# Kernel optimization log

Measured on AMD Instinct MI355X. Metric: run time of the kernel, lower is better.

Reference implementation:

```python
import jax, jax.numpy as jnp
import numpy as np

N, E, F, H, G = 50000, 1600000, 128, 128, 64
EPS = 1e-5  # BatchNorm eps


def setup_inputs() -> dict:
    key = jax.random.key(0)
    ks = jax.random.split(key, 16)
    x = jax.random.normal(ks[0], (N, F), dtype=jnp.float32)
    edge_index = jax.random.randint(ks[1], (2, E), 0, N, dtype=jnp.int64)
    batch = jnp.sort(jax.random.randint(ks[2], (N,), 0, G, dtype=jnp.int64))
    inp = {
        'x': x, 'edge_index': edge_index, 'batch': batch,
        'W1': jax.random.normal(ks[3], (F, H), dtype=jnp.float32) / np.sqrt(F),
        'b1': jnp.zeros((H,), jnp.float32),
        'bn1_gamma': jax.random.uniform(ks[4], (H,), jnp.float32, 0.5, 1.5),
        'bn1_beta': jax.random.normal(ks[5], (H,), jnp.float32) * 0.1,
        'bn1_mean': jax.random.normal(ks[6], (H,), jnp.float32) * 0.1,
        'bn1_var': jax.random.uniform(ks[7], (H,), jnp.float32, 0.5, 1.5),
        'W2': jax.random.normal(ks[8], (H, H), dtype=jnp.float32) / np.sqrt(H),
        'b2': jnp.zeros((H,), jnp.float32),
        'bn2_gamma': jax.random.uniform(ks[9], (H,), jnp.float32, 0.5, 1.5),
        'bn2_beta': jax.random.normal(ks[10], (H,), jnp.float32) * 0.1,
        'bn2_mean': jax.random.normal(ks[11], (H,), jnp.float32) * 0.1,
        'bn2_var': jax.random.uniform(ks[12], (H,), jnp.float32, 0.5, 1.5),
        'att_w': jax.random.normal(ks[13], (H, 1), dtype=jnp.float32) / np.sqrt(H),
        'cls_w': jax.random.normal(ks[14], (1, H), dtype=jnp.float32) / np.sqrt(H),
        'cls_b': jnp.zeros((1,), jnp.float32),
    }
    return inp


def gcn_conv(h, W, b, src, dst, n):
    # PyG GCNConv: linear, add self-loops, symmetric D^{-1/2}(A+I)D^{-1/2} aggregation, bias.
    hw = h @ W                                   # [n, H]
    loops = jnp.arange(n, dtype=src.dtype)
    s = jnp.concatenate([src, loops])
    d = jnp.concatenate([dst, loops])
    deg = jax.ops.segment_sum(jnp.ones_like(d, dtype=hw.dtype), d, num_segments=n)
    dis = jnp.where(deg > 0, jax.lax.rsqrt(deg), 0.0)
    norm = dis[s] * dis[d]                       # [E+n]
    msgs = hw[s] * norm[:, None]                 # gather + scale (memory-bound)
    return jax.ops.segment_sum(msgs, d, num_segments=n) + b


def batch_norm(h, gamma, beta, mean, var):
    return (h - mean) * gamma * jax.lax.rsqrt(var + EPS) + beta


def reference(x, edge_index, batch, W1, b1, bn1_gamma, bn1_beta, bn1_mean, bn1_var,
              W2, b2, bn2_gamma, bn2_beta, bn2_mean, bn2_var, att_w, cls_w, cls_b):
    n = x.shape[0]
    src, dst = edge_index[0], edge_index[1]
    # eval mode: dropout and edge-dropout are no-ops; BN uses running stats
    h = gcn_conv(x, W1, b1, src, dst, n)
    h = jax.nn.relu(batch_norm(h, bn1_gamma, bn1_beta, bn1_mean, bn1_var))
    h = gcn_conv(h, W2, b2, src, dst, n)
    h = jax.nn.relu(batch_norm(h, bn2_gamma, bn2_beta, bn2_mean, bn2_var))
    att = jax.nn.sigmoid(h @ att_w)              # [n, 1]
    g = jax.ops.segment_sum(h * att, batch, num_segments=G)  # [G, H]
    logits = g @ cls_w.T + cls_b                 # [G, 1]
    return logits, att
```

## Files before the change

### kernel.cpp

```cpp
#include <hip/hip_runtime.h>
#include <math.h>

#define NN 50000
#define HID 128
#define NG 64
#define BN_EPS 1e-5f

typedef __attribute__((ext_vector_type(8))) short short8;
typedef __attribute__((ext_vector_type(4))) float f32x4;

__device__ inline unsigned pack_bf2(float a, float b) {
    union { float f; unsigned u; } ua, ub;
    ua.f = a; ub.f = b;
    unsigned x = ua.u, y = ub.u;
    x += 0x7fffu + ((x >> 16) & 1u);
    y += 0x7fffu + ((y >> 16) & 1u);
    return (x >> 16) | (y & 0xffff0000u);
}
__device__ inline unsigned short bf16_1(float x) {
    union { float f; unsigned u; } v;
    v.f = x;
    unsigned r = v.u + 0x7fffu + ((v.u >> 16) & 1u);
    return (unsigned short)(r >> 16);
}
__device__ inline float2 unpack_bf2(unsigned v) {
    union { unsigned u; float f; } a, b;
    a.u = v << 16;
    b.u = v & 0xffff0000u;
    return make_float2(a.f, b.f);
}

#define NBKT 256
#define ETILE 8192
#define CAP   8192

__global__ __launch_bounds__(256) void k_distribute(const int* __restrict__ src,
                                                    const int* __restrict__ dst,
                                                    int* __restrict__ bcurP,
                                                    unsigned* __restrict__ bpacked,
                                                    const float* __restrict__ W1,
                                                    const float* __restrict__ W2,
                                                    unsigned short* __restrict__ wt1,
                                                    unsigned short* __restrict__ wt2,
                                                    int etiles, int E, int K) {
    if ((int)blockIdx.x >= etiles) {
        int b2 = blockIdx.x - etiles;
        int k = b2 & 127;
        const float* W = (b2 < 128) ? W1 : W2;
        unsigned short* wt = (b2 < 128) ? wt1 : wt2;
        int c = threadIdx.x;
        if (c < 128) wt[c * 128 + k] = bf16_1(W[k * 128 + c]);
        return;
    }
    __shared__ int h[NBKT];
    int t = threadIdx.x;
    h[t] = 0;
    __syncthreads();
    int base = blockIdx.x * ETILE;
    for (int i = 0; i < ETILE / 256; ++i) {
        int e = base + i * 256 + t;
        if (e < E) atomicAdd(&h[dst[e] / K], 1);
    }
    __syncthreads();
    int c = h[t];
    int my = (c > 0) ? atomicAdd(&bcurP[t * 16], c) : 0;
    __syncthreads();
    h[t] = my;
    __syncthreads();
    for (int i = 0; i < ETILE / 256; ++i) {
        int e = base + i * 256 + t;
        if (e < E) {
            int d = dst[e];
            int bkt = d / K;
            int p = atomicAdd(&h[bkt], 1);
            bpacked[(size_t)bkt * CAP + p] = ((unsigned)d << 16) | (unsigned)src[e];
        }
    }
}

__global__ __launch_bounds__(256) void k_bucket_csr(const unsigned* __restrict__ bpacked,
                                                    const int* __restrict__ bcurP,
                                                    int* __restrict__ row_ptr,
                                                    int* __restrict__ degA,
                                                    float* __restrict__ dis,
                                                    int* __restrict__ col_idx,
                                                    const float* __restrict__ cls_b,
                                                    float* __restrict__ logits,
                                                    int n, int K) {
    __shared__ int cnt[NBKT];
    __shared__ int sA[NBKT];
    __shared__ int cur[NBKT];
    int t = threadIdx.x;
    int b = blockIdx.x;
    if (b == 0 && t < NG) logits[t] = cls_b[0];
    int node0 = b * K;
    int nn = n - node0;
    if (nn > K) nn = K;
    if (nn < 0) nn = 0;
    int e0 = b * CAP;
    int e1 = e0 + bcurP[b * 16];
    cnt[t] = 0;
    __syncthreads();
    for (int e = e0 + t; e < e1; e += 256) {
        int ld = (int)(bpacked[e] >> 16) - node0;
        atomicAdd(&cnt[ld], 1);
    }
    __syncthreads();
    int c = cnt[t];
    sA[t] = c;
    __syncthreads();
    for (int off = 1; off < NBKT; off <<= 1) {
        int v = (t >= off) ? sA[t - off] : 0;
        __syncthreads();
        sA[t] += v;
        __syncthreads();
    }
    int rp = e0 + sA[t] - c;
    cur[t] = rp;
    if (t < nn) {
        row_ptr[node0 + t] = rp;
        degA[node0 + t] = c;
        dis[node0 + t] = rsqrtf((float)(c + 1));
    }
    __syncthreads();
    for (int e = e0 + t; e < e1; e += 256) {
        unsigned v = bpacked[e];
        int ld = (int)(v >> 16) - node0;
        int p = atomicAdd(&cur[ld], 1);
        col_idx[p] = (int)(v & 0xFFFFu);
    }
}


#define ASTR 136

__global__ __launch_bounds__(256) void k_gemm_mfma(const void* __restrict__ inp,
                                                   const unsigned short* __restrict__ wt,
                                                   const float* __restrict__ dis,
                                                   unsigned short* __restrict__ outb,
                                                   int n, int fmt) {
    __shared__ unsigned short A[64][ASTR];
    int t = threadIdx.x;
    int row0 = blockIdx.x * 64;

    if (fmt == 0) {
        const float* in = (const float*)inp;
        #pragma unroll
        for (int i = 0; i < 8; ++i) {
            int idx = t + i * 256;
            int r = idx >> 5;
            int c4 = (idx & 31) * 4;
            float4 v = make_float4(0.f, 0.f, 0.f, 0.f);
            if (row0 + r < n) v = *(const float4*)&in[(size_t)(row0 + r) * 128 + c4];
            uint2 p;
            p.x = pack_bf2(v.x, v.y);
            p.y = pack_bf2(v.z, v.w);
            *(uint2*)&A[r][c4] = p;
        }
    } else {
        const unsigned short* in = (const unsigned short*)inp;
        #pragma unroll
        for (int i = 0; i < 4; ++i) {
            int idx = t + i * 256;
            int r = idx >> 4;
            int c8 = (idx & 15) * 8;
            uint4 v = make_uint4(0, 0, 0, 0);
            if (row0 + r < n) v = *(const uint4*)&in[(size_t)(row0 + r) * 128 + c8];
            *(uint4*)&A[r][c8] = v;
        }
    }
    __syncthreads();

    int lane = t & 63;
    int wave = t >> 6;
    int m = lane & 15;
    int quad = lane >> 4;
    int r0 = wave * 16;

    short8 a[4];
    #pragma unroll
    for (int kt = 0; kt < 4; ++kt)
        a[kt] = *(const short8*)&A[r0 + m][kt * 32 + quad * 8];

    f32x4 acc[8];
    #pragma unroll
    for (int ct = 0; ct < 8; ++ct) acc[ct] = (f32x4){0.f, 0.f, 0.f, 0.f};

    short8 bcur[4], bnxt[4];
    {
        const unsigned short* wb = &wt[(size_t)m * 128 + quad * 8];
        #pragma unroll
        for (int kt = 0; kt < 4; ++kt) bcur[kt] = *(const short8*)(wb + kt * 32);
    }
    #pragma unroll
    for (int ct = 0; ct < 8; ++ct) {
        if (ct < 7) {
            const unsigned short* wb = &wt[(size_t)((ct + 1) * 16 + m) * 128 + quad * 8];
            #pragma unroll
            for (int kt = 0; kt < 4; ++kt) bnxt[kt] = *(const short8*)(wb + kt * 32);
        }
        #pragma unroll
        for (int kt = 0; kt < 4; ++kt)
            acc[ct] = __builtin_amdgcn_mfma_f32_16x16x32_bf16(a[kt], bcur[kt], acc[ct], 0, 0, 0);
        #pragma unroll
        for (int kt = 0; kt < 4; ++kt) bcur[kt] = bnxt[kt];
    }

    int gr = row0 + r0 + quad * 4;
    float ds[4];
    #pragma unroll
    for (int reg = 0; reg < 4; ++reg)
        ds[reg] = (gr + reg < n) ? dis[gr + reg] : 0.f;

    __syncthreads();
    #pragma unroll
    for (int ct = 0; ct < 8; ++ct) {
        int col = ct * 16 + m;
        #pragma unroll
        for (int reg = 0; reg < 4; ++reg)
            A[r0 + quad * 4 + reg][col] = bf16_1(acc[ct][reg] * ds[reg]);
    }
    __syncthreads();
    #pragma unroll
    for (int i = 0; i < 4; ++i) {
        int idx = t + i * 256;
        int r = idx >> 4;
        int c8 = (idx & 15) * 8;
        int grow = row0 + r;
        if (grow < n)
            *(uint4*)&outb[(size_t)grow * 128 + c8] = *(const uint4*)&A[r][c8];
    }
}


__device__ inline void gather4wide(const unsigned short* __restrict__ hwsb,
                                   const int* __restrict__ col_idx,
                                   int e0, int deg, int md,
                                   int sl, int part, bool active,
                                   float* acc8) {
    int cidx = (active && sl < deg) ? col_idx[e0 + sl] : 0;
    for (int it0 = 0; it0 < md; it0 += 16) {
        int nx = it0 + 16;
        int cidx_next = (active && (nx + sl) < deg && nx < md) ? col_idx[e0 + nx + sl] : 0;
        uint4 vv[16];
        #pragma unroll
        for (int j = 0; j < 16; ++j) {
            int s = __shfl(cidx, (part << 4) + j);
            vv[j] = (it0 + j < deg)
                        ? *(const uint4*)(hwsb + ((size_t)s << 7) + (sl << 3))
                        : make_uint4(0, 0, 0, 0);
        }
        #pragma unroll
        for (int j = 0; j < 16; ++j) {
            const unsigned* w = (const unsigned*)&vv[j];
            #pragma unroll
            for (int i2 = 0; i2 < 4; ++i2) {
                float2 f = unpack_bf2(w[i2]);
                acc8[2 * i2]     += f.x;
                acc8[2 * i2 + 1] += f.y;
            }
        }
        cidx = cidx_next;
    }
}


__global__ __launch_bounds__(256) void k_agg_bn_relu(const unsigned short* __restrict__ hwsb,
                                                     const int* __restrict__ row_ptr,
                                                     const int* __restrict__ degA,
                                                     const int* __restrict__ col_idx,
                                                     const float* __restrict__ dis,
                                                     const float* __restrict__ bias,
                                                     const float* __restrict__ gamma,
                                                     const float* __restrict__ beta,
                                                     const float* __restrict__ mean,
                                                     const float* __restrict__ var,
                                                     unsigned short* __restrict__ outh, int n) {
    int t = threadIdx.x;
    int wave = t >> 6, lane = t & 63;
    int sl = lane & 15, part = lane >> 4;
    int d = blockIdx.x * 16 + wave * 4 + part;
    bool active = (d < n);
    int e0 = 0, deg = 0;
    if (active) {
        e0 = row_ptr[d];
        deg = degA[d];
    }
    int md = deg;
    md = max(md, __shfl_xor(md, 16));
    md = max(md, __shfl_xor(md, 32));

    float acc8[8] = {0, 0, 0, 0, 0, 0, 0, 0};
    gather4wide(hwsb, col_idx, e0, deg, md, sl, part, active, acc8);
    if (!active) return;

    {
        uint4 v = *(const uint4*)(hwsb + ((size_t)d << 7) + (sl << 3));
        const unsigned* w = (const unsigned*)&v;
        #pragma unroll
        for (int i2 = 0; i2 < 4; ++i2) {
            float2 f = unpack_bf2(w[i2]);
            acc8[2 * i2]     += f.x;
            acc8[2 * i2 + 1] += f.y;
        }
    }
    float dd = dis[d];
    int f0 = sl << 3;
    unsigned outw[4];
    #pragma unroll
    for (int i2 = 0; i2 < 4; ++i2) {
        int f = f0 + 2 * i2;
        float2 bv = *(const float2*)&bias[f];
        float2 gm = *(const float2*)&gamma[f];
        float2 bt = *(const float2*)&beta[f];
        float2 mn = *(const float2*)&mean[f];
        float2 vr = *(const float2*)&var[f];
        float vx = acc8[2 * i2] * dd + bv.x;
        float vy = acc8[2 * i2 + 1] * dd + bv.y;
        float sx = gm.x * rsqrtf(vr.x + BN_EPS);
        float sy = gm.y * rsqrtf(vr.y + BN_EPS);
        float rx = fmaxf((vx - mn.x) * sx + bt.x, 0.f);
        float ry = fmaxf((vy - mn.y) * sy + bt.y, 0.f);
        outw[i2] = pack_bf2(rx, ry);
    }
    *(uint4*)(outh + ((size_t)d << 7) + (sl << 3)) = *(uint4*)outw;
}


__global__ __launch_bounds__(256) void k_agg2_att_logit(const unsigned short* __restrict__ hwsb,
                                                        const int* __restrict__ row_ptr,
                                                        const int* __restrict__ degA,
                                                        const int* __restrict__ col_idx,
                                                        const float* __restrict__ dis,
                                                        const float* __restrict__ bias,
                                                        const float* __restrict__ gamma,
                                                        const float* __restrict__ beta,
                                                        const float* __restrict__ mean,
                                                        const float* __restrict__ var,
                                                        const int* __restrict__ batch,
                                                        const float* __restrict__ att_w,
                                                        const float* __restrict__ cls_w,
                                                        float* __restrict__ att_out,
                                                        float* __restrict__ logits, int n) {
    __shared__ int   sg[16];
    __shared__ float sv[16];
    int t = threadIdx.x;
    int wave = t >> 6, lane = t & 63;
    int sl = lane & 15, part = lane >> 4;
    int d = blockIdx.x * 16 + wave * 4 + part;
    bool active = (d < n);
    int e0 = 0, deg = 0;
    if (active) {
        e0 = row_ptr[d];
        deg = degA[d];
    }
    int md = deg;
    md = max(md, __shfl_xor(md, 16));
    md = max(md, __shfl_xor(md, 32));

    float acc8[8] = {0, 0, 0, 0, 0, 0, 0, 0};
    gather4wide(hwsb, col_idx, e0, deg, md, sl, part, active, acc8);

    int g = -1;
    float contrib = 0.f;
    float p = 0.f, q = 0.f;
    if (active) {
        uint4 v = *(const uint4*)(hwsb + ((size_t)d << 7) + (sl << 3));
        const unsigned* w = (const unsigned*)&v;
        #pragma unroll
        for (int i2 = 0; i2 < 4; ++i2) {
            float2 f = unpack_bf2(w[i2]);
            acc8[2 * i2]     += f.x;
            acc8[2 * i2 + 1] += f.y;
        }
        float dd = dis[d];
        int f0 = sl << 3;
        #pragma unroll
        for (int i2 = 0; i2 < 4; ++i2) {
            int f = f0 + 2 * i2;
            float2 bv = *(const float2*)&bias[f];
            float2 gm = *(const float2*)&gamma[f];
            float2 bt = *(const float2*)&beta[f];
            float2 mn = *(const float2*)&mean[f];
            float2 vr = *(const float2*)&var[f];
            float vx = acc8[2 * i2] * dd + bv.x;
            float vy = acc8[2 * i2 + 1] * dd + bv.y;
            float sx = gm.x * rsqrtf(vr.x + BN_EPS);
            float sy = gm.y * rsqrtf(vr.y + BN_EPS);
            float rx = fmaxf((vx - mn.x) * sx + bt.x, 0.f);
            float ry = fmaxf((vy - mn.y) * sy + bt.y, 0.f);
            float2 aw = *(const float2*)&att_w[f];
            float2 cw = *(const float2*)&cls_w[f];
            p += rx * aw.x + ry * aw.y;
            q += rx * cw.x + ry * cw.y;
        }
    }
    #pragma unroll
    for (int off = 1; off < 16; off <<= 1) {
        p += __shfl_xor(p, off);
        q += __shfl_xor(q, off);
    }
    if (active) {
        float a = 1.f / (1.f + expf(-p));
        if (sl == 0) att_out[d] = a;
        g = batch[d];
        contrib = a * q;
    }
    if (sl == 0) {
        sg[wave * 4 + part] = g;
        sv[wave * 4 + part] = contrib;
    }
    __syncthreads();
    if (t == 0) {
        int cur = -1;
        float acc = 0.f;
        #pragma unroll
        for (int i = 0; i < 16; ++i) {
            int gi = sg[i];
            if (gi < 0) continue;
            if (gi != cur) {
                if (cur >= 0) atomicAdd(&logits[cur], acc);
                cur = gi;
                acc = 0.f;
            }
            acc += sv[i];
        }
        if (cur >= 0) atomicAdd(&logits[cur], acc);
    }
}


extern "C" void kernel_launch(void* const* d_in, const int* in_sizes, int n_in,
                              void* d_out, int out_size, void* d_ws, size_t ws_size,
                              hipStream_t stream) {
    const float* x   = (const float*)d_in[0];
    const int*   ei  = (const int*)d_in[1];
    const int*   bat = (const int*)d_in[2];
    const float* W1  = (const float*)d_in[3];
    const float* b1  = (const float*)d_in[4];
    const float* g1  = (const float*)d_in[5];
    const float* bt1 = (const float*)d_in[6];
    const float* mn1 = (const float*)d_in[7];
    const float* vr1 = (const float*)d_in[8];
    const float* W2  = (const float*)d_in[9];
    const float* b2  = (const float*)d_in[10];
    const float* g2  = (const float*)d_in[11];
    const float* bt2 = (const float*)d_in[12];
    const float* mn2 = (const float*)d_in[13];
    const float* vr2 = (const float*)d_in[14];
    const float* attw = (const float*)d_in[15];
    const float* clsw = (const float*)d_in[16];
    const float* clsb = (const float*)d_in[17];

    int E = in_sizes[1] / 2;
    int n = in_sizes[2];
    const int* src = ei;
    const int* dst = ei + E;
    int K = (n + NBKT - 1) / NBKT;

    char* ws = (char*)d_ws;
    auto alloc = [&](size_t bytes) {
        void* p = (void*)ws;
        ws += (bytes + 255) & ~(size_t)255;
        return p;
    };
    int*            bcurP   = (int*)alloc(NBKT * 16 * 4);
    unsigned*       bpacked = (unsigned*)alloc((size_t)NBKT * CAP * 4);
    int*            row_ptr = (int*)alloc((size_t)n * 4);
    int*            degA    = (int*)alloc((size_t)n * 4);
    int*            col_idx = (int*)alloc((size_t)NBKT * CAP * 4);
    float*          dis     = (float*)alloc((size_t)n * 4);
    unsigned short* hwsb    = (unsigned short*)alloc((size_t)n * 128 * 2);
    unsigned short* h1b     = (unsigned short*)alloc((size_t)n * 128 * 2);
    unsigned short* wt1     = (unsigned short*)alloc(128 * 128 * 2);
    unsigned short* wt2     = (unsigned short*)alloc(128 * 128 * 2);

    float* out = (float*)d_out;
    int etiles = (E + ETILE - 1) / ETILE;
    int gb = (n + 63) / 64;
    int ab = (n + 15) / 16;

    hipMemsetAsync(bcurP, 0, NBKT * 16 * 4, stream);
    k_distribute<<<etiles + 256, 256, 0, stream>>>(src, dst, bcurP, bpacked,
                                                   W1, W2, wt1, wt2, etiles, E, K);
    k_bucket_csr<<<NBKT, 256, 0, stream>>>(bpacked, bcurP, row_ptr, degA, dis,
                                           col_idx, clsb, out, n, K);

    k_gemm_mfma<<<gb, 256, 0, stream>>>(x, wt1, dis, hwsb, n, 0);
    k_agg_bn_relu<<<ab, 256, 0, stream>>>(hwsb, row_ptr, degA, col_idx, dis,
                                          b1, g1, bt1, mn1, vr1, h1b, n);
    k_gemm_mfma<<<gb, 256, 0, stream>>>(h1b, wt2, dis, hwsb, n, 1);
    k_agg2_att_logit<<<ab, 256, 0, stream>>>(hwsb, row_ptr, degA, col_idx, dis,
                                             b2, g2, bt2, mn2, vr2, bat, attw, clsw,
                                             out + NG, out, n);
}
```

Baseline: 309.0 us.

## Fuse layer-1 aggregation with layer-2 GEMM in one kernel

The layer-1 aggregation+BN+ReLU kernel now stages its 16-row output tile in shared memory and immediately multiplies it by W2 with MFMA, writing the dis-scaled layer-2 features directly. This removes the h1 intermediate round trip through global memory and one kernel launch. The cost is that W2 is reloaded from global or L2 by every 16-row block rather than amortised over 64-row tiles, plus extra barriers and shared-memory use in the gather kernel.

```diff
diff --git a/kernel.cpp b/kernel.cpp
--- a/kernel.cpp
+++ b/kernel.cpp
@@ -134,40 +134,25 @@
 
 #define ASTR 136
 
-__global__ __launch_bounds__(256) void k_gemm_mfma(const void* __restrict__ inp,
+__global__ __launch_bounds__(256) void k_gemm_mfma(const float* __restrict__ in,
                                                    const unsigned short* __restrict__ wt,
                                                    const float* __restrict__ dis,
-                                                   unsigned short* __restrict__ outb,
-                                                   int n, int fmt) {
+                                                   unsigned short* __restrict__ outb, int n) {
     __shared__ unsigned short A[64][ASTR];
     int t = threadIdx.x;
     int row0 = blockIdx.x * 64;
 
-    if (fmt == 0) {
-        const float* in = (const float*)inp;
-        #pragma unroll
-        for (int i = 0; i < 8; ++i) {
-            int idx = t + i * 256;
-            int r = idx >> 5;
-            int c4 = (idx & 31) * 4;
-            float4 v = make_float4(0.f, 0.f, 0.f, 0.f);
-            if (row0 + r < n) v = *(const float4*)&in[(size_t)(row0 + r) * 128 + c4];
-            uint2 p;
-            p.x = pack_bf2(v.x, v.y);
-            p.y = pack_bf2(v.z, v.w);
-            *(uint2*)&A[r][c4] = p;
-        }
-    } else {
-        const unsigned short* in = (const unsigned short*)inp;
-        #pragma unroll
-        for (int i = 0; i < 4; ++i) {
-            int idx = t + i * 256;
-            int r = idx >> 4;
-            int c8 = (idx & 15) * 8;
-            uint4 v = make_uint4(0, 0, 0, 0);
-            if (row0 + r < n) v = *(const uint4*)&in[(size_t)(row0 + r) * 128 + c8];
-            *(uint4*)&A[r][c8] = v;
-        }
+    #pragma unroll
+    for (int i = 0; i < 8; ++i) {
+        int idx = t + i * 256;
+        int r = idx >> 5;
+        int c4 = (idx & 31) * 4;
+        float4 v = make_float4(0.f, 0.f, 0.f, 0.f);
+        if (row0 + r < n) v = *(const float4*)&in[(size_t)(row0 + r) * 128 + c4];
+        uint2 p;
+        p.x = pack_bf2(v.x, v.y);
+        p.y = pack_bf2(v.z, v.w);
+        *(uint2*)&A[r][c4] = p;
     }
     __syncthreads();
 
@@ -265,17 +250,20 @@
 }
 
 
-__global__ __launch_bounds__(256) void k_agg_bn_relu(const unsigned short* __restrict__ hwsb,
-                                                     const int* __restrict__ row_ptr,
-                                                     const int* __restrict__ degA,
-                                                     const int* __restrict__ col_idx,
-                                                     const float* __restrict__ dis,
-                                                     const float* __restrict__ bias,
-                                                     const float* __restrict__ gamma,
-                                                     const float* __restrict__ beta,
-                                                     const float* __restrict__ mean,
-                                                     const float* __restrict__ var,
-                                                     unsigned short* __restrict__ outh, int n) {
+__global__ __launch_bounds__(256) void k_agg1_gemm2(const unsigned short* __restrict__ hwsb1,
+                                                    const int* __restrict__ row_ptr,
+                                                    const int* __restrict__ degA,
+                                                    const int* __restrict__ col_idx,
+                                                    const float* __restrict__ dis,
+                                                    const float* __restrict__ bias,
+                                                    const float* __restrict__ gamma,
+                                                    const float* __restrict__ beta,
+                                                    const float* __restrict__ mean,
+                                                    const float* __restrict__ var,
+                                                    const unsigned short* __restrict__ wt2,
+                                                    unsigned short* __restrict__ hwsb2, int n) {
+    __shared__ unsigned short H1[16][ASTR];
+    __shared__ unsigned short C2[16][ASTR];
     int t = threadIdx.x;
     int wave = t >> 6, lane = t & 63;
     int sl = lane & 15, part = lane >> 4;
@@ -291,11 +279,11 @@
     md = max(md, __shfl_xor(md, 32));
 
     float acc8[8] = {0, 0, 0, 0, 0, 0, 0, 0};
-    gather4wide(hwsb, col_idx, e0, deg, md, sl, part, active, acc8);
-    if (!active) return;
-
-    {
-        uint4 v = *(const uint4*)(hwsb + ((size_t)d << 7) + (sl << 3));
+    gather4wide(hwsb1, col_idx, e0, deg, md, sl, part, active, acc8);
+
+    unsigned outw[4] = {0, 0, 0, 0};
+    if (active) {
+        uint4 v = *(const uint4*)(hwsb1 + ((size_t)d << 7) + (sl << 3));
         const unsigned* w = (const unsigned*)&v;
         #pragma unroll
         for (int i2 = 0; i2 < 4; ++i2) {
@@ -303,27 +291,69 @@
             acc8[2 * i2]     += f.x;
             acc8[2 * i2 + 1] += f.y;
         }
-    }
-    float dd = dis[d];
-    int f0 = sl << 3;
-    unsigned outw[4];
-    #pragma unroll
-    for (int i2 = 0; i2 < 4; ++i2) {
-        int f = f0 + 2 * i2;
-        float2 bv = *(const float2*)&bias[f];
-        float2 gm = *(const float2*)&gamma[f];
-        float2 bt = *(const float2*)&beta[f];
-        float2 mn = *(const float2*)&mean[f];
-        float2 vr = *(const float2*)&var[f];
-        float vx = acc8[2 * i2] * dd + bv.x;
-        float vy = acc8[2 * i2 + 1] * dd + bv.y;
-        float sx = gm.x * rsqrtf(vr.x + BN_EPS);
-        float sy = gm.y * rsqrtf(vr.y + BN_EPS);
-        float rx = fmaxf((vx - mn.x) * sx + bt.x, 0.f);
-        float ry = fmaxf((vy - mn.y) * sy + bt.y, 0.f);
-        outw[i2] = pack_bf2(rx, ry);
-    }
-    *(uint4*)(outh + ((size_t)d << 7) + (sl << 3)) = *(uint4*)outw;
+        float dd = dis[d];
+        int f0 = sl << 3;
+        #pragma unroll
+        for (int i2 = 0; i2 < 4; ++i2) {
+            int f = f0 + 2 * i2;
+            float2 bv = *(const float2*)&bias[f];
+            float2 gm = *(const float2*)&gamma[f];
+            float2 bt = *(const float2*)&beta[f];
+            float2 mn = *(const float2*)&mean[f];
+            float2 vr = *(const float2*)&var[f];
+            float vx = acc8[2 * i2] * dd + bv.x;
+            float vy = acc8[2 * i2 + 1] * dd + bv.y;
+            float sx = gm.x * rsqrtf(vr.x + BN_EPS);
+            float sy = gm.y * rsqrtf(vr.y + BN_EPS);
+            float rx = fmaxf((vx - mn.x) * sx + bt.x, 0.f);
+            float ry = fmaxf((vy - mn.y) * sy + bt.y, 0.f);
+            outw[i2] = pack_bf2(rx, ry);
+        }
+    }
+    int local = wave * 4 + part;
+    *(uint4*)&H1[local][sl << 3] = *(uint4*)outw;
+    __syncthreads();
+
+    int m = sl;
+    int quad = part;
+    short8 a2[4];
+    #pragma unroll
+    for (int kt = 0; kt < 4; ++kt)
+        a2[kt] = *(const short8*)&H1[m][kt * 32 + quad * 8];
+
+    f32x4 acc2[2];
+    acc2[0] = (f32x4){0.f, 0.f, 0.f, 0.f};
+    acc2[1] = (f32x4){0.f, 0.f, 0.f, 0.f};
+    #pragma unroll
+    for (int i = 0; i < 2; ++i) {
+        int ct = wave * 2 + i;
+        const unsigned short* wb = &wt2[(size_t)(ct * 16 + m) * 128 + quad * 8];
+        #pragma unroll
+        for (int kt = 0; kt < 4; ++kt) {
+            short8 b = *(const short8*)(wb + kt * 32);
+            acc2[i] = __builtin_amdgcn_mfma_f32_16x16x32_bf16(a2[kt], b, acc2[i], 0, 0, 0);
+        }
+    }
+    int gr = blockIdx.x * 16 + quad * 4;
+    float ds2[4];
+    #pragma unroll
+    for (int reg = 0; reg < 4; ++reg)
+        ds2[reg] = (gr + reg < n) ? dis[gr + reg] : 0.f;
+    #pragma unroll
+    for (int i = 0; i < 2; ++i) {
+        int col = (wave * 2 + i) * 16 + m;
+        #pragma unroll
+        for (int reg = 0; reg < 4; ++reg)
+            C2[quad * 4 + reg][col] = bf16_1(acc2[i][reg] * ds2[reg]);
+    }
+    __syncthreads();
+    {
+        int r = t >> 4;
+        int c8 = (t & 15) * 8;
+        int grow = blockIdx.x * 16 + r;
+        if (grow < n)
+            *(uint4*)&hwsb2[(size_t)grow * 128 + c8] = *(const uint4*)&C2[r][c8];
+    }
 }
 
 
@@ -470,8 +500,8 @@
     int*            degA    = (int*)alloc((size_t)n * 4);
     int*            col_idx = (int*)alloc((size_t)NBKT * CAP * 4);
     float*          dis     = (float*)alloc((size_t)n * 4);
-    unsigned short* hwsb    = (unsigned short*)alloc((size_t)n * 128 * 2);
-    unsigned short* h1b     = (unsigned short*)alloc((size_t)n * 128 * 2);
+    unsigned short* hwsb1   = (unsigned short*)alloc((size_t)n * 128 * 2);
+    unsigned short* hwsb2   = (unsigned short*)alloc((size_t)n * 128 * 2);
     unsigned short* wt1     = (unsigned short*)alloc(128 * 128 * 2);
     unsigned short* wt2     = (unsigned short*)alloc(128 * 128 * 2);
 
@@ -486,11 +516,10 @@
     k_bucket_csr<<<NBKT, 256, 0, stream>>>(bpacked, bcurP, row_ptr, degA, dis,
                                            col_idx, clsb, out, n, K);
 
-    k_gemm_mfma<<<gb, 256, 0, stream>>>(x, wt1, dis, hwsb, n, 0);
-    k_agg_bn_relu<<<ab, 256, 0, stream>>>(hwsb, row_ptr, degA, col_idx, dis,
-                                          b1, g1, bt1, mn1, vr1, h1b, n);
-    k_gemm_mfma<<<gb, 256, 0, stream>>>(h1b, wt2, dis, hwsb, n, 1);
-    k_agg2_att_logit<<<ab, 256, 0, stream>>>(hwsb, row_ptr, degA, col_idx, dis,
+    k_gemm_mfma<<<gb, 256, 0, stream>>>(x, wt1, dis, hwsb1, n);
+    k_agg1_gemm2<<<ab, 256, 0, stream>>>(hwsb1, row_ptr, degA, col_idx, dis,
+                                         b1, g1, bt1, mn1, vr1, wt2, hwsb2, n);
+    k_agg2_att_logit<<<ab, 256, 0, stream>>>(hwsb2, row_ptr, degA, col_idx, dis,
                                              b2, g2, bt2, mn2, vr2, bat, attw, clsw,
                                              out + NG, out, n);
 }
```

Measured after the change: 293.7 us. 5.0% less time.
